# Kernel tuning notes

Hardware: AMD Instinct MI355X
Metric: run time of the kernel (lower is better)

## Reference

```python
import jax, jax.numpy as jnp
import numpy as np

B, S, L, D = 32, 8, 128, 768
A, T = 10, 8
VOCAB = 1000


def setup_inputs() -> dict:
    key = jax.random.key(0)
    k1, k2, k3, k4, k5 = jax.random.split(key, 5)
    sentence_ids = jax.random.randint(k1, (B, S, L), 0, VOCAB)
    sentence_attention_masks = jnp.ones((B, S, L), dtype=jnp.float32)
    # precomputed sum of last 4 BERT hidden layers (backbone excluded)
    sentence_embeddings = jax.random.normal(k2, (B, S, L, D), dtype=jnp.float32)
    predicate_ids = jax.random.randint(k3, (B, S, A, T), 0, VOCAB)
    arg0_ids = jax.random.randint(k4, (B, S, A, T), 0, VOCAB)
    arg1_ids = jax.random.randint(k5, (B, S, A, T), 0, VOCAB)
    return {
        "sentence_ids": sentence_ids,
        "sentence_attention_masks": sentence_attention_masks,
        "sentence_embeddings": sentence_embeddings,
        "predicate_ids": predicate_ids,
        "arg0_ids": arg0_ids,
        "arg1_ids": arg1_ids,
    }


def _mean_pool(emb, mask):
    # emb: [b,s,l,d], mask: [b,s,l] -> [b,s,d]
    masked_sum = jnp.einsum('bsld,bsl->bsd', emb, mask)
    counts = jnp.clip(mask.sum(-1, keepdims=True), 1, None)
    return masked_sum / counts


def _arg_embedding(arg_ids, sentence_ids, emb):
    # arg_ids: [b,s,a,t] int, sentence_ids: [b,s,l] int, emb: [b,s,l,d]
    # match[b,s,a,t,l] = sentence token l equals arg token t (and arg token != 0)
    match = (sentence_ids[:, :, None, None, :] == arg_ids[..., None]) & (arg_ids[..., None] != 0)
    mf = match.astype(emb.dtype)
    counts = mf.sum(-1)                                   # [b,s,a,t]
    summed = jnp.einsum('bsatl,bsld->bsatd', mf, emb)      # [b,s,a,t,d]
    avg = summed / jnp.maximum(counts, 1.0)[..., None]
    has = counts > 0                                       # [b,s,a,t]
    t_dim = arg_ids.shape[-1]
    # original loop overwrites per token -> keep the LAST token with a match
    last = (t_dim - 1) - jnp.argmax(has[..., ::-1], axis=-1)  # [b,s,a]
    sel = jnp.take_along_axis(avg, last[..., None, None], axis=3)[:, :, :, 0, :]
    valid = has.any(-1)                                    # [b,s,a]
    return jnp.where(valid[..., None], sel, jnp.zeros((), emb.dtype))


def reference(sentence_ids, sentence_attention_masks, sentence_embeddings,
              predicate_ids, arg0_ids, arg1_ids):
    sentence_embeddings_avg = _mean_pool(sentence_embeddings, sentence_attention_masks)
    predicate_embeddings = _arg_embedding(predicate_ids, sentence_ids, sentence_embeddings)
    arg0_embeddings = _arg_embedding(arg0_ids, sentence_ids, sentence_embeddings)
    arg1_embeddings = _arg_embedding(arg1_ids, sentence_ids, sentence_embeddings)
    return (sentence_embeddings_avg, predicate_embeddings, arg0_embeddings, arg1_embeddings)
```

## Files before the change

kernel.cpp:

```cpp
#include <hip/hip_runtime.h>

#define Bq 32
#define Sq 8
#define Lq 128
#define Dq 768
#define Aq 10
#define Tq 8

typedef float f32x4 __attribute__((ext_vector_type(4)));

constexpr int D4    = Dq / 4;
constexpr int NBS   = Bq * Sq;
constexpr int NBSA  = NBS * Aq;
constexpr int NPOOL = NBS * 3;
constexpr int NARG  = NBS * 3;

__global__ __launch_bounds__(64) void srl_fused_k(
    const int* __restrict__ sids, const float* __restrict__ mask,
    const float* __restrict__ emb, const int* __restrict__ pred,
    const int* __restrict__ a0, const int* __restrict__ a1,
    float* __restrict__ out)
{
    int bid  = blockIdx.x;
    int lane = threadIdx.x;

    if (bid < NPOOL) {
        int bs    = bid / 3;
        int third = bid - bs * 3;

        __shared__ float marr[Lq];
        float m0 = mask[(size_t)bs * Lq + lane];
        float m1 = mask[(size_t)bs * Lq + 64 + lane];
        marr[lane]      = m0;
        marr[64 + lane] = m1;
        float mv = m0 + m1;
        for (int off = 32; off > 0; off >>= 1)
            mv += __shfl_xor(mv, off);
        float inv = 1.0f / fmaxf(mv, 1.0f);
        __syncthreads();

        const f32x4* eb = (const f32x4*)emb +
                          (size_t)bs * Lq * D4 + third * 64 + lane;
        f32x4 acc = {0.f, 0.f, 0.f, 0.f};
#pragma unroll 16
        for (int l = 0; l < Lq; ++l) {
            float m = marr[l];
            f32x4 v = eb[(size_t)l * D4];
            acc += v * m;
        }
        f32x4 r = acc * inv;
        ((f32x4*)out)[(size_t)bs * D4 + third * 64 + lane] = r;
        return;
    }

    int j   = bid - NPOOL;
    int bs  = j / 3;
    int set = j - bs * 3;
    const int* ids = (set == 0) ? pred : ((set == 1) ? a0 : a1);

    int s0 = sids[(size_t)bs * Lq + lane];
    int s1 = sids[(size_t)bs * Lq + 64 + lane];

    const f32x4* eb = (const f32x4*)emb + (size_t)bs * Lq * D4;

    for (int a = 0; a < Aq; ++a) {
        int bsa = bs * Aq + a;
        int idv = (lane < Tq) ? ids[(size_t)bsa * Tq + lane] : 0;

        unsigned long long B0 = 0, B1 = 0;
        int ccount = 0;
#pragma unroll
        for (int t = Tq - 1; t >= 0; --t) {
            if (ccount == 0) {
                int idt = __shfl(idv, t);
                if (idt != 0) {
                    unsigned long long b0 = __ballot(s0 == idt);
                    unsigned long long b1 = __ballot(s1 == idt);
                    int c = (int)(__popcll(b0) + __popcll(b1));
                    if (c > 0) { B0 = b0; B1 = b1; ccount = c; }
                }
            }
        }

        f32x4 acc0 = {0.f, 0.f, 0.f, 0.f};
        f32x4 acc1 = acc0, acc2 = acc0;
        unsigned long long b = B0;
        while (b) {
            int l = (int)__builtin_ctzll(b); b &= b - 1;
            acc0 += eb[(size_t)l * D4 + lane];
            acc1 += eb[(size_t)l * D4 + 64 + lane];
            acc2 += eb[(size_t)l * D4 + 128 + lane];
        }
        b = B1;
        while (b) {
            int l = (int)__builtin_ctzll(b) + 64; b &= b - 1;
            acc0 += eb[(size_t)l * D4 + lane];
            acc1 += eb[(size_t)l * D4 + 64 + lane];
            acc2 += eb[(size_t)l * D4 + 128 + lane];
        }

        float inv = (ccount > 0) ? 1.0f / (float)ccount : 0.0f;
        f32x4* o4 = (f32x4*)out +
                    ((size_t)NBS + (size_t)set * NBSA + bsa) * D4;
        o4[lane]       = acc0 * inv;
        o4[64 + lane]  = acc1 * inv;
        o4[128 + lane] = acc2 * inv;
    }
}

extern "C" void kernel_launch(void* const* d_in, const int* in_sizes, int n_in,
                              void* d_out, int out_size, void* d_ws, size_t ws_size,
                              hipStream_t stream) {
    const int*   sids = (const int*)d_in[0];
    const float* mask = (const float*)d_in[1];
    const float* emb  = (const float*)d_in[2];
    const int*   pred = (const int*)d_in[3];
    const int*   a0   = (const int*)d_in[4];
    const int*   a1   = (const int*)d_in[5];
    float* out = (float*)d_out;

    srl_fused_k<<<NPOOL + NARG, 64, 0, stream>>>(sids, mask, emb,
                                                 pred, a0, a1, out);
}
```

Measured before the change: 26.78 us.

## Fuse arg gathers into mean-pool streaming pass via per-token match bitmasks

Instead of separate blocks for pooling and for arg gathers, each block now streams its slice of the embedding once and both mean-pools it and scatters each row into 30 shared-memory accumulators, selected by a per-token bitmask built up front from ballots. This removes the second read of the embedding rows by the arg blocks and halves the grid. In exchange, every block now repeats all 30 arg match computations, which is redundant work done three times per (b,s), and holds 30 KB of LDS accumulators, which may lower occupancy. Loads and stores are also switched to nontemporal.

```diff
diff --git a/kernel.cpp b/kernel.cpp
--- a/kernel.cpp
+++ b/kernel.cpp
@@ -9,11 +9,10 @@
 
 typedef float f32x4 __attribute__((ext_vector_type(4)));
 
-constexpr int D4    = Dq / 4;
-constexpr int NBS   = Bq * Sq;
-constexpr int NBSA  = NBS * Aq;
-constexpr int NPOOL = NBS * 3;
-constexpr int NARG  = NBS * 3;
+constexpr int D4   = Dq / 4;
+constexpr int NBS  = Bq * Sq;
+constexpr int NBSA = NBS * Aq;
+constexpr int NJ   = 3 * Aq;
 
 __global__ __launch_bounds__(64) void srl_fused_k(
     const int* __restrict__ sids, const float* __restrict__ mask,
@@ -23,88 +22,85 @@
 {
     int bid  = blockIdx.x;
     int lane = threadIdx.x;
+    int bs    = bid / 3;
+    int third = bid - bs * 3;
 
-    if (bid < NPOOL) {
-        int bs    = bid / 3;
-        int third = bid - bs * 3;
+    __shared__ f32x4        accA[NJ][64];
+    __shared__ float        marr[Lq];
+    __shared__ unsigned int mbits[Lq];
+    __shared__ float        scl[NJ];
 
-        __shared__ float marr[Lq];
-        float m0 = mask[(size_t)bs * Lq + lane];
-        float m1 = mask[(size_t)bs * Lq + 64 + lane];
-        marr[lane]      = m0;
-        marr[64 + lane] = m1;
-        float mv = m0 + m1;
-        for (int off = 32; off > 0; off >>= 1)
-            mv += __shfl_xor(mv, off);
-        float inv = 1.0f / fmaxf(mv, 1.0f);
-        __syncthreads();
+#pragma unroll
+    for (int j = 0; j < NJ; ++j) accA[j][lane] = (f32x4){0.f, 0.f, 0.f, 0.f};
 
-        const f32x4* eb = (const f32x4*)emb +
-                          (size_t)bs * Lq * D4 + third * 64 + lane;
-        f32x4 acc = {0.f, 0.f, 0.f, 0.f};
-#pragma unroll 16
-        for (int l = 0; l < Lq; ++l) {
-            float m = marr[l];
-            f32x4 v = eb[(size_t)l * D4];
-            acc += v * m;
-        }
-        f32x4 r = acc * inv;
-        ((f32x4*)out)[(size_t)bs * D4 + third * 64 + lane] = r;
-        return;
-    }
-
-    int j   = bid - NPOOL;
-    int bs  = j / 3;
-    int set = j - bs * 3;
-    const int* ids = (set == 0) ? pred : ((set == 1) ? a0 : a1);
+    float m0 = mask[(size_t)bs * Lq + lane];
+    float m1 = mask[(size_t)bs * Lq + 64 + lane];
+    marr[lane]      = m0;
+    marr[64 + lane] = m1;
+    float mv = m0 + m1;
+    for (int off = 32; off > 0; off >>= 1) mv += __shfl_xor(mv, off);
+    float invm = 1.0f / fmaxf(mv, 1.0f);
 
     int s0 = sids[(size_t)bs * Lq + lane];
     int s1 = sids[(size_t)bs * Lq + 64 + lane];
 
-    const f32x4* eb = (const f32x4*)emb + (size_t)bs * Lq * D4;
+    unsigned int mb0 = 0, mb1 = 0;
+#pragma unroll
+    for (int set = 0; set < 3; ++set) {
+        const int* ids = (set == 0) ? pred : ((set == 1) ? a0 : a1);
+        for (int a = 0; a < Aq; ++a) {
+            int bsa = bs * Aq + a;
+            int idv = (lane < Tq) ? ids[(size_t)bsa * Tq + lane] : 0;
 
-    for (int a = 0; a < Aq; ++a) {
-        int bsa = bs * Aq + a;
-        int idv = (lane < Tq) ? ids[(size_t)bsa * Tq + lane] : 0;
-
-        unsigned long long B0 = 0, B1 = 0;
-        int ccount = 0;
+            unsigned long long B0 = 0, B1 = 0;
+            int cc = 0;
 #pragma unroll
-        for (int t = Tq - 1; t >= 0; --t) {
-            if (ccount == 0) {
-                int idt = __shfl(idv, t);
-                if (idt != 0) {
-                    unsigned long long b0 = __ballot(s0 == idt);
-                    unsigned long long b1 = __ballot(s1 == idt);
-                    int c = (int)(__popcll(b0) + __popcll(b1));
-                    if (c > 0) { B0 = b0; B1 = b1; ccount = c; }
+            for (int t = Tq - 1; t >= 0; --t) {
+                if (cc == 0) {
+                    int idt = __shfl(idv, t);
+                    if (idt != 0) {
+                        unsigned long long b0 = __ballot(s0 == idt);
+                        unsigned long long b1 = __ballot(s1 == idt);
+                        int c = (int)(__popcll(b0) + __popcll(b1));
+                        if (c > 0) { B0 = b0; B1 = b1; cc = c; }
+                    }
                 }
             }
+            int j = set * Aq + a;
+            mb0 |= (unsigned int)((B0 >> lane) & 1ull) << j;
+            mb1 |= (unsigned int)((B1 >> lane) & 1ull) << j;
+            if (lane == 0) scl[j] = (cc > 0) ? 1.0f / (float)cc : 0.0f;
         }
+    }
+    mbits[lane]      = mb0;
+    mbits[64 + lane] = mb1;
+    __syncthreads();
 
-        f32x4 acc0 = {0.f, 0.f, 0.f, 0.f};
-        f32x4 acc1 = acc0, acc2 = acc0;
-        unsigned long long b = B0;
-        while (b) {
-            int l = (int)__builtin_ctzll(b); b &= b - 1;
-            acc0 += eb[(size_t)l * D4 + lane];
-            acc1 += eb[(size_t)l * D4 + 64 + lane];
-            acc2 += eb[(size_t)l * D4 + 128 + lane];
+    const f32x4* eb = (const f32x4*)emb +
+                      (size_t)bs * Lq * D4 + third * 64 + lane;
+    f32x4 accP = {0.f, 0.f, 0.f, 0.f};
+#pragma unroll 8
+    for (int l = 0; l < Lq; ++l) {
+        f32x4 v = __builtin_nontemporal_load(&eb[(size_t)l * D4]);
+        accP += v * marr[l];
+        unsigned int mb = mbits[l];
+        while (mb) {
+            int j = (int)__builtin_ctz(mb); mb &= mb - 1;
+            accA[j][lane] += v;
         }
-        b = B1;
-        while (b) {
-            int l = (int)__builtin_ctzll(b) + 64; b &= b - 1;
-            acc0 += eb[(size_t)l * D4 + lane];
-            acc1 += eb[(size_t)l * D4 + 64 + lane];
-            acc2 += eb[(size_t)l * D4 + 128 + lane];
-        }
+    }
 
-        float inv = (ccount > 0) ? 1.0f / (float)ccount : 0.0f;
-        f32x4* o4 = (f32x4*)out +
-                    ((size_t)NBS + (size_t)set * NBSA + bsa) * D4;
-        o4[lane]       = acc0 * inv;
-        o4[64 + lane]  = acc1 * inv;
-        o4[128 + lane] = acc2 * inv;
+    __builtin_nontemporal_store(accP * invm,
+        (f32x4*)out + (size_t)bs * D4 + third * 64 + lane);
+
+#pragma unroll
+    for (int j = 0; j < NJ; ++j) {
+        int set = j / Aq, a = j - set * Aq;
+        int bsa = bs * Aq + a;
+        f32x4 r = accA[j][lane] * scl[j];
+        __builtin_nontemporal_store(r,
+            (f32x4*)out + ((size_t)NBS + (size_t)set * NBSA + bsa) * D4 +
+            third * 64 + lane);
     }
 }
 
@@ -119,6 +115,6 @@
     const int*   a1   = (const int*)d_in[5];
     float* out = (float*)d_out;
 
-    srl_fused_k<<<NPOOL + NARG, 64, 0, stream>>>(sids, mask, emb,
-                                                 pred, a0, a1, out);
+    srl_fused_k<<<NBS * 3, 64, 0, stream>>>(sids, mask, emb,
+                                            pred, a0, a1, out);
 }
```

After: 57.73 us. 116% more time.
